# Kernel tuning notes

Hardware: AMD Instinct MI355X
Metric: run time of the kernel (lower is better)

Reference implementation:

```python
import jax, jax.numpy as jnp
import numpy as np
import math

B, S, D = 4, 4096, 1024
H = 16
HD = D // H          # head_dim = 64
M = 256              # nb_features (random projection dim)


def _orthogonal_gaussian(key, m, d):
    # FAVOR+ orthogonal random features: blocks of d orthogonal rows,
    # each row rescaled to a chi-distributed norm (norm of a d-dim gaussian).
    n_blocks = int(math.ceil(m / d))
    keys = jax.random.split(key, n_blocks + 1)
    blocks = []
    for i in range(n_blocks):
        g = jax.random.normal(keys[i], (d, d), dtype=jnp.float32)
        q, _ = jnp.linalg.qr(g)
        blocks.append(q.T)
    W = jnp.concatenate(blocks, axis=0)[:m]  # [m, d]
    norms = jnp.linalg.norm(
        jax.random.normal(keys[-1], (m, d), dtype=jnp.float32), axis=1, keepdims=True)
    return W * norms


def _softmax_kernel(x, proj, is_query, eps=1e-4):
    # x: [b,h,s,d]; proj: [m,d]. Standard FAVOR+ positive softmax features.
    d = x.shape[-1]
    ratio = proj.shape[0] ** -0.5
    x = x * (d ** -0.25)
    u = jnp.einsum('bhsd,md->bhsm', x, proj)  # projection
    diag = 0.5 * jnp.sum(x * x, axis=-1, keepdims=True)  # [b,h,s,1]
    if is_query:
        stab = jnp.max(u, axis=-1, keepdims=True)
    else:
        stab = jnp.max(u, axis=(-1, -2), keepdims=True)
    return ratio * (jnp.exp(u - diag - stab) + eps)


def performer_attention(Q, K, V, mask, proj):
    # Q,K,V: [b,h,s,d], mask: [b,s]
    scale = HD ** -0.25
    m4 = mask[:, None, :, None]
    Qs = Q * scale
    Ks = K * scale * m4
    Vs = V * m4
    q_prime = _softmax_kernel(Qs, proj, is_query=True)   # [b,h,s,m]
    k_prime = _softmax_kernel(Ks, proj, is_query=False)  # [b,h,s,m]
    # linear attention: O(s*m*d)
    kv = jnp.einsum('bhsm,bhsd->bhmd', k_prime, Vs)      # [b,h,m,d]
    z = 1.0 / (jnp.einsum('bhsm,bhm->bhs', q_prime, jnp.sum(k_prime, axis=2)) + 1e-6)
    out = jnp.einsum('bhsm,bhmd->bhsd', q_prime, kv) * z[..., None]
    return out


def setup_inputs() -> dict:
    key = jax.random.key(0)
    ks = jax.random.split(key, 9)
    X = jax.random.normal(ks[0], (B, S, D), dtype=jnp.float32)
    mask = jnp.ones((B, S), dtype=jnp.float32)
    s = D ** -0.5
    Wq = jax.random.normal(ks[1], (D, D), dtype=jnp.float32) * s
    bq = jnp.zeros((D,), dtype=jnp.float32)
    Wk = jax.random.normal(ks[2], (D, D), dtype=jnp.float32) * s
    bk = jnp.zeros((D,), dtype=jnp.float32)
    Wv = jax.random.normal(ks[3], (D, D), dtype=jnp.float32) * s
    bv = jnp.zeros((D,), dtype=jnp.float32)
    proj = _orthogonal_gaussian(ks[4], M, HD)
    return {"X": X, "mask": mask, "Wq": Wq, "bq": bq, "Wk": Wk, "bk": bk,
            "Wv": Wv, "bv": bv, "proj": proj}


def _split_heads(x):
    b, s, _ = x.shape
    return x.reshape(b, s, H, HD).transpose(0, 2, 1, 3)


def reference(X, mask, Wq, bq, Wk, bk, Wv, bv, proj):
    Q = _split_heads(X @ Wq + bq)
    K = _split_heads(X @ Wk + bk)
    V = _split_heads(X @ Wv + bv)
    attn = performer_attention(Q, K, V, mask, proj)  # [b,h,s,hd]
    out = attn.transpose(0, 2, 1, 3).reshape(B, S, D)
    return out
```

## Files before the change

### kernel.cpp

```cpp
#include <hip/hip_runtime.h>
#include <stdint.h>

#define DEVI static __device__ __forceinline__

typedef unsigned short u16;
typedef unsigned int u32;
typedef __attribute__((ext_vector_type(8))) short short8;
typedef __attribute__((ext_vector_type(4))) float f32x4;
typedef __attribute__((ext_vector_type(4))) unsigned short ushort4_t;

#define BB 4
#define SS 4096
#define DD 1024
#define HH 16
#define HDD 64
#define MM 256
#define BHN 64

DEVI u16 f2bf(float f) {
    u32 u = __float_as_uint(f);
    u += 0x7fffu + ((u >> 16) & 1u);
    return (u16)(u >> 16);
}
DEVI float bf2f(u16 h) { return __uint_as_float(((u32)h) << 16); }

typedef __attribute__((address_space(1))) const unsigned int as1_u32;
typedef __attribute__((address_space(3))) unsigned int as3_u32;
DEVI void load_lds16(const void* g, void* lds) {
    __builtin_amdgcn_global_load_lds((as1_u32*)g, (as3_u32*)lds, 16, 0, 0);
}


__global__ void conv_bf16(const float* __restrict__ src, u16* __restrict__ dst, int n4) {
    int i = blockIdx.x * 256 + threadIdx.x;
    if (i < n4) {
        float4 v = reinterpret_cast<const float4*>(src)[i];
        ushort4_t o = { f2bf(v.x), f2bf(v.y), f2bf(v.z), f2bf(v.w) };
        reinterpret_cast<ushort4_t*>(dst)[i] = o;
    }
}

__global__ void conv_w(const float* __restrict__ Wq, const float* __restrict__ Wk,
                       const float* __restrict__ Wv, u16* __restrict__ Wt) {
    __shared__ float tile[64][65];
    const int jt = blockIdx.x, kt = blockIdx.y;
    const float* src = (jt < 16) ? Wq : (jt < 32) ? Wk : Wv;
    const int j0 = (jt & 15) * 64, k0 = kt * 64;
    const int t = threadIdx.x;
    for (int i = 0; i < 16; ++i) {
        int lin = t + i * 256;
        int kl = lin >> 6, jl = lin & 63;
        tile[kl][jl] = src[(size_t)(k0 + kl) * DD + j0 + jl];
    }
    __syncthreads();
    const int jg0 = jt * 64;
    for (int i = 0; i < 16; ++i) {
        int lin = t + i * 256;
        int jl = lin >> 6, kl = lin & 63;
        Wt[(size_t)(jg0 + jl) * DD + k0 + kl] = f2bf(tile[kl][jl]);
    }
}

__global__ __launch_bounds__(512, 2) void gemm1_big(
    const u16* __restrict__ Xbf, const u16* __restrict__ Wt,
    const float* __restrict__ bq, const float* __restrict__ bk, const float* __restrict__ bv,
    const float* __restrict__ mask,
    u16* __restrict__ Qh, u16* __restrict__ Kh, u16* __restrict__ Vt,
    float* __restrict__ dq, float* __restrict__ dk)
{
    extern __shared__ __align__(16) char smem[];
    const int tid = threadIdx.x, l = tid & 63, wv = tid >> 6;
    const int wm = wv >> 2, wn = wv & 3;
    const int bid = blockIdx.x;
    const int xcd = bid & 7, i6 = bid >> 3;
    const int bx = xcd * 8 + i6 / 12, by = i6 % 12;
    const int row0 = bx * 256, col0 = by * 256;

    const int srow = tid >> 3;
    const int scol = ((tid & 7) ^ (srow & 7)) * 8;

    #define ABUF(p) ((char*)smem + (p) * 32768)
    #define BBUF(p) ((char*)smem + 65536 + (p) * 32768)
    #define STA(p, kt, r) load_lds16(Xbf + (size_t)(row0 + (r)*64 + srow) * DD + (kt)*64 + scol, \
                                     ABUF(p) + (r)*8192 + wv*1024)
    #define STB(p, kt, r) load_lds16(Wt + (size_t)(col0 + (r)*64 + srow) * DD + (kt)*64 + scol, \
                                     BBUF(p) + (r)*8192 + wv*1024)

    STA(0,0,0); STA(0,0,1); STA(0,0,2); STA(0,0,3);
    STB(0,0,0); STB(0,0,1); STB(0,0,2); STB(0,0,3);
    asm volatile("s_waitcnt vmcnt(0)" ::: "memory");
    __builtin_amdgcn_s_barrier();
    __builtin_amdgcn_sched_barrier(0);

    f32x4 acc[8][4] = {};
    const int arow_b = wm * 128 + (l & 15);
    const int brow_b = wn * 64 + (l & 15);
    const int cb_b = (l >> 4) * 16;
    const int lx = (l & 7) << 4;

    for (int kt = 0; kt < 16; ++kt) {
        const int p = kt & 1, pn = p ^ 1;
        const bool more = (kt + 1) < 16;
        short8 bfr[4][2];
#pragma unroll
        for (int q = 0; q < 4; ++q) {
            if (more) {
                if (q == 0)      { STA(pn, kt + 1, 0); STA(pn, kt + 1, 1); }
                else if (q == 1) { STA(pn, kt + 1, 2); STA(pn, kt + 1, 3); }
                else if (q == 2) { STB(pn, kt + 1, 0); STB(pn, kt + 1, 1); }
                else             { STB(pn, kt + 1, 2); STB(pn, kt + 1, 3); }
            }
            if (q == 0) {
#pragma unroll
                for (int nf = 0; nf < 4; ++nf) {
                    const int br = brow_b + nf * 16;
#pragma unroll
                    for (int ks = 0; ks < 2; ++ks)
                        bfr[nf][ks] = *(const short8*)(BBUF(p) + br * 128 + ((cb_b + ks * 64) ^ lx));
                }
            }
            short8 a[2][2];
#pragma unroll
            for (int i = 0; i < 2; ++i) {
                const int ar = arow_b + (q * 2 + i) * 16;
#pragma unroll
                for (int ks = 0; ks < 2; ++ks)
                    a[i][ks] = *(const short8*)(ABUF(p) + ar * 128 + ((cb_b + ks * 64) ^ lx));
            }
            __builtin_amdgcn_s_setprio(1);
#pragma unroll
            for (int i = 0; i < 2; ++i)
#pragma unroll
                for (int nf = 0; nf < 4; ++nf) {
                    acc[q*2+i][nf] = __builtin_amdgcn_mfma_f32_16x16x32_bf16(a[i][0], bfr[nf][0], acc[q*2+i][nf], 0, 0, 0);
                    acc[q*2+i][nf] = __builtin_amdgcn_mfma_f32_16x16x32_bf16(a[i][1], bfr[nf][1], acc[q*2+i][nf], 0, 0, 0);
                }
            __builtin_amdgcn_s_setprio(0);
            __builtin_amdgcn_sched_barrier(0);
        }
        asm volatile("s_waitcnt vmcnt(0)" ::: "memory");
        __builtin_amdgcn_s_barrier();
        __builtin_amdgcn_sched_barrier(0);
    }

    const int region = by >> 2;
    const int h = ((by & 3) << 2) + wn;
    const int rg = row0 + wm * 128;
    const int b = rg >> 12;
    const int sb = rg & 4095;
    const size_t bh = (size_t)(b * HH + h);
    const int dd = l & 15;
    const int jbase = ((by & 3) << 8) + wn * 64;

    if (region == 0) {
        float bias[4];
#pragma unroll
        for (int nf = 0; nf < 4; ++nf) bias[nf] = bq[jbase + nf * 16 + dd];
#pragma unroll
        for (int mf = 0; mf < 8; ++mf) {
            float ds4[4];
#pragma unroll
            for (int g = 0; g < 4; ++g) {
                const int s = sb + mf * 16 + ((l >> 4) << 2) + g;
                float dsum = 0.f;
#pragma unroll
                for (int nf = 0; nf < 4; ++nf) {
                    u16 hv = f2bf((acc[mf][nf][g] + bias[nf]) * 0.125f);
                    Qh[(bh * SS + s) * HDD + nf * 16 + dd] = hv;
                    float fv = bf2f(hv);
                    dsum += fv * fv;
                }
                dsum += __shfl_xor(dsum, 1);
                dsum += __shfl_xor(dsum, 2);
                dsum += __shfl_xor(dsum, 4);
                dsum += __shfl_xor(dsum, 8);
                ds4[g] = 0.5f * dsum;
            }
            if (dd == 0)
                *(float4*)(dq + bh * SS + sb + mf * 16 + ((l >> 4) << 2)) =
                    make_float4(ds4[0], ds4[1], ds4[2], ds4[3]);
        }
    } else if (region == 1) {
        float bias[4];
#pragma unroll
        for (int nf = 0; nf < 4; ++nf) bias[nf] = bk[jbase + nf * 16 + dd];
#pragma unroll
        for (int mf = 0; mf < 8; ++mf) {
            float ds4[4];
#pragma unroll
            for (int g = 0; g < 4; ++g) {
                const int s = sb + mf * 16 + ((l >> 4) << 2) + g;
                const float m = mask[b * SS + s];
                float dsum = 0.f;
#pragma unroll
                for (int nf = 0; nf < 4; ++nf) {
                    u16 hv = f2bf((acc[mf][nf][g] + bias[nf]) * m * 0.125f);
                    Kh[(bh * SS + s) * HDD + nf * 16 + dd] = hv;
                    float fv = bf2f(hv);
                    dsum += fv * fv;
                }
                dsum += __shfl_xor(dsum, 1);
                dsum += __shfl_xor(dsum, 2);
                dsum += __shfl_xor(dsum, 4);
                dsum += __shfl_xor(dsum, 8);
                ds4[g] = 0.5f * dsum;
            }
            if (dd == 0)
                *(float4*)(dk + bh * SS + sb + mf * 16 + ((l >> 4) << 2)) =
                    make_float4(ds4[0], ds4[1], ds4[2], ds4[3]);
        }
    } else {
        float bias[4];
#pragma unroll
        for (int nf = 0; nf < 4; ++nf) bias[nf] = bv[jbase + nf * 16 + dd];
#pragma unroll
        for (int mf = 0; mf < 8; ++mf) {
            const int s0 = sb + mf * 16 + ((l >> 4) << 2);
#pragma unroll
            for (int nf = 0; nf < 4; ++nf) {
                ushort4_t pk;
#pragma unroll
                for (int g = 0; g < 4; ++g) {
                    const float m = mask[b * SS + s0 + g];
                    pk[g] = f2bf((acc[mf][nf][g] + bias[nf]) * m);
                }
                *(ushort4_t*)(Vt + (bh * HDD + nf * 16 + dd) * SS + s0) = pk;
            }
        }
    }
    #undef ABUF
    #undef BBUF
    #undef STA
    #undef STB
}

__global__ __launch_bounds__(256, 2) void kv_fused(
    const u16* __restrict__ Kh, const u16* __restrict__ Vt,
    const u16* __restrict__ projb, const float* __restrict__ dk,
    float* __restrict__ kv_part, float* __restrict__ ksum_part,
    float* __restrict__ vsum_part, float* __restrict__ lstab)
{
    extern __shared__ __align__(16) char ksm[];
    #define KLDS(b) ((char*)ksm + (b) * 8192)
    #define VLDS(b) ((char*)ksm + 24576 + (b) * 8192)
    u16* Kp = (u16*)((char*)ksm + 49152);
    const int tid = threadIdx.x, l = tid & 63, wv = tid >> 6;
    const int ck = blockIdx.x, bh = blockIdx.y;
    short8 pb[4][2];
#pragma unroll
    for (int nf = 0; nf < 4; ++nf)
#pragma unroll
        for (int ks = 0; ks < 2; ++ks)
            pb[nf][ks] = *(const short8*)(projb + (wv * 64 + nf * 16 + (l & 15)) * HDD + ks * 32 + (l >> 4) * 8);
    const size_t sbase = (size_t)bh * SS + ck * 512;

    #define KSTAGE(buf, it8) do { \
        const int s0_ = (it8) * 64; \
        _Pragma("unroll") \
        for (int c = 0; c < 2; ++c) { \
            const int rb = wv * 16 + c * 8; \
            const int r = rb + (l >> 3); \
            const int sc = ((l & 7) ^ (r & 7)) * 8; \
            load_lds16(Kh + (sbase + s0_ + r) * HDD + sc, KLDS(buf) + rb * 128); \
        } \
    } while (0)
    #define VSTAGE(buf, it8) do { \
        const int s0_ = (it8) * 64; \
        _Pragma("unroll") \
        for (int c = 0; c < 2; ++c) { \
            const int rb = wv * 16 + c * 8; \
            const int r = rb + (l >> 3); \
            const int sc = ((l & 7) ^ (r & 7)) * 8; \
            load_lds16(Vt + ((size_t)bh * HDD + r) * SS + ck * 512 + s0_ + sc, VLDS(buf) + rb * 128); \
        } \
    } while (0)

    float wmax = -3.0e38f;
    KSTAGE(0, 0);
    for (int it = 0; it < 8; ++it) {
        if (it + 1 < 8) {
            KSTAGE((it + 1) % 3, it + 1);
            asm volatile("s_waitcnt vmcnt(2)" ::: "memory");
        } else {
            asm volatile("s_waitcnt vmcnt(0)" ::: "memory");
        }
        __syncthreads();
        const int bs = it % 3;
#pragma unroll
        for (int sf = 0; sf < 4; ++sf) {
            const int s = sf * 16 + (l & 15);
            f32x4 u4[4] = {};
#pragma unroll
            for (int ks = 0; ks < 2; ++ks) {
                short8 ak = *(const short8*)(KLDS(bs) + s * 128 + ((ks * 64 + (l >> 4) * 16) ^ ((s & 7) << 4)));
#pragma unroll
                for (int nf = 0; nf < 4; ++nf)
                    u4[nf] = __builtin_amdgcn_mfma_f32_16x16x32_bf16(ak, pb[nf][ks], u4[nf], 0, 0, 0);
            }
#pragma unroll
            for (int nf = 0; nf < 4; ++nf)
#pragma unroll
                for (int g = 0; g < 4; ++g) wmax = fmaxf(wmax, u4[nf][g]);
        }
    }
#pragma unroll
    for (int o = 1; o < 64; o <<= 1) wmax = fmaxf(wmax, __shfl_xor(wmax, o));
    if (l == 0) lstab[((size_t)ck * BHN + bh) * 4 + wv] = wmax;
    const float stab = wmax;

    f32x4 acc[4][4] = {};
    float ksc[4] = {0.f, 0.f, 0.f, 0.f};
    float vsc[4] = {0.f, 0.f, 0.f, 0.f};
    KSTAGE(0, 0); VSTAGE(0, 0);
    for (int it = 0; it < 8; ++it) {
        if (it + 1 < 8) {
            KSTAGE((it + 1) % 3, it + 1);
            VSTAGE((it + 1) % 3, it + 1);
            asm volatile("s_waitcnt vmcnt(4)" ::: "memory");
        } else {
            asm volatile("s_waitcnt vmcnt(0)" ::: "memory");
        }
        __syncthreads();
        const int bs = it % 3;
        const int s0 = it * 64;
#pragma unroll
        for (int sf = 0; sf < 4; ++sf) {
            const int s = sf * 16 + (l & 15);
            f32x4 u4[4] = {};
#pragma unroll
            for (int ks = 0; ks < 2; ++ks) {
                short8 ak = *(const short8*)(KLDS(bs) + s * 128 + ((ks * 64 + (l >> 4) * 16) ^ ((s & 7) << 4)));
#pragma unroll
                for (int nf = 0; nf < 4; ++nf)
                    u4[nf] = __builtin_amdgcn_mfma_f32_16x16x32_bf16(ak, pb[nf][ks], u4[nf], 0, 0, 0);
            }
            const int srow = sf * 16 + (l >> 4) * 4;
            const float4 dkv = *(const float4*)(dk + sbase + s0 + srow);
#pragma unroll
            for (int nf = 0; nf < 4; ++nf) {
                const int m = wv * 64 + nf * 16 + (l & 15);
                u16 h0 = f2bf(__expf(u4[nf][0] - dkv.x - stab));
                u16 h1 = f2bf(__expf(u4[nf][1] - dkv.y - stab));
                u16 h2 = f2bf(__expf(u4[nf][2] - dkv.z - stab));
                u16 h3 = f2bf(__expf(u4[nf][3] - dkv.w - stab));
                ksc[nf] += bf2f(h0) + bf2f(h1) + bf2f(h2) + bf2f(h3);
                uint2 w; w.x = (u32)h0 | ((u32)h1 << 16); w.y = (u32)h2 | ((u32)h3 << 16);
                *(uint2*)((char*)Kp + m * 128 + ((srow * 2) ^ ((m & 7) << 4))) = w;
            }
        }
        __syncthreads();
#pragma unroll
        for (int ks = 0; ks < 2; ++ks) {
            short8 am[4], bv8[4];
#pragma unroll
            for (int mf = 0; mf < 4; ++mf) {
                const int m = wv * 64 + mf * 16 + (l & 15);
                am[mf] = *(const short8*)((const char*)Kp + m * 128 + ((ks * 64 + (l >> 4) * 16) ^ ((m & 7) << 4)));
            }
#pragma unroll
            for (int nf = 0; nf < 4; ++nf) {
                const int d = nf * 16 + (l & 15);
                bv8[nf] = *(const short8*)(VLDS(bs) + d * 128 + ((ks * 64 + (l >> 4) * 16) ^ ((d & 7) << 4)));
                float vs = 0.f;
#pragma unroll
                for (int e = 0; e < 8; ++e) vs += bf2f((u16)bv8[nf][e]);
                vsc[nf] += vs;
            }
#pragma unroll
            for (int mf = 0; mf < 4; ++mf)
#pragma unroll
                for (int nf = 0; nf < 4; ++nf)
                    acc[mf][nf] = __builtin_amdgcn_mfma_f32_16x16x32_bf16(am[mf], bv8[nf], acc[mf][nf], 0, 0, 0);
        }
    }
    const size_t pbase = (size_t)ck * BHN + bh;
#pragma unroll
    for (int nf = 0; nf < 4; ++nf) {
        float v = ksc[nf];
        v += __shfl_xor(v, 16);
        v += __shfl_xor(v, 32);
        if (l < 16) ksum_part[pbase * MM + wv * 64 + nf * 16 + l] = v;
        float w = vsc[nf];
        w += __shfl_xor(w, 16);
        w += __shfl_xor(w, 32);
        if (wv == 0 && l < 16) vsum_part[pbase * HDD + nf * 16 + l] = w;
    }
#pragma unroll
    for (int mf = 0; mf < 4; ++mf)
#pragma unroll
        for (int nf = 0; nf < 4; ++nf)
            *(f32x4*)(kv_part + (pbase * HDD + nf * 16 + (l & 15)) * MM + wv * 64 + mf * 16 + (l >> 4) * 4) = acc[mf][nf];
    #undef KLDS
    #undef VLDS
    #undef KSTAGE
    #undef VSTAGE
}

__global__ void reduceB3(const float* __restrict__ kv_part, const float* __restrict__ ksum_part,
                         const float* __restrict__ vsum_part, const float* __restrict__ lstab,
                         u16* __restrict__ Bmat) {
    __shared__ float f[8][4];
    const int bh = blockIdx.x, n = blockIdx.y, t = threadIdx.x;
    if (t < 32) {
        float lv = lstab[((size_t)(t >> 2) * BHN + bh) * 4 + (t & 3)];
        float g = lv;
#pragma unroll
        for (int o = 1; o < 32; o <<= 1) g = fmaxf(g, __shfl_xor(g, o));
        f[t >> 2][t & 3] = __expf(lv - g);
    }
    __syncthreads();
    const int grp = t >> 6;
    float s = 0.f;
    if (n < 64) {
        float vsg = 0.f;
#pragma unroll
        for (int ck = 0; ck < 8; ++ck) {
            vsg += vsum_part[((size_t)ck * BHN + bh) * HDD + n];
            s += kv_part[(((size_t)ck * BHN + bh) * HDD + n) * MM + t] * f[ck][grp];
        }
        s = 0.0625f * (s + 1e-4f * vsg);
    } else if (n == 64) {
#pragma unroll
        for (int ck = 0; ck < 8; ++ck)
            s += ksum_part[((size_t)ck * BHN + bh) * MM + t] * f[ck][grp];
        s = 0.0625f * (s + 1e-4f * 4096.0f);
    }
    Bmat[((size_t)bh * 80 + n) * MM + t] = (n <= 64) ? f2bf(s) : (u16)0;
}

__global__ __launch_bounds__(256) void out_fused(
    const u16* __restrict__ Qh, const u16* __restrict__ projb,
    const float* __restrict__ dq, const u16* __restrict__ Bmat,
    float* __restrict__ out)
{
    __shared__ __align__(16) u16 Qlds[64 * 64];
    __shared__ __align__(16) u16 qlds[64 * 256];
    __shared__ float red[4][64];
    const int tid = threadIdx.x, l = tid & 63, wv = tid >> 6;
    const int rt = blockIdx.x, bh = blockIdx.y;
    const size_t srowbase = (size_t)bh * SS + rt * 64;
#pragma unroll
    for (int c = 0; c < 2; ++c) {
        const int rb = wv * 16 + c * 8;
        const int r = rb + (l >> 3);
        load_lds16(Qh + (srowbase + r) * HDD + (((l & 7) ^ (r & 7)) * 8), (char*)Qlds + rb * 128);
    }
    short8 pa[4][2];
#pragma unroll
    for (int mf = 0; mf < 4; ++mf)
#pragma unroll
        for (int ks = 0; ks < 2; ++ks)
            pa[mf][ks] = *(const short8*)(projb + (wv * 64 + mf * 16 + (l & 15)) * HDD + ks * 32 + (l >> 4) * 8);
    __syncthreads();
    f32x4 u[4][4] = {};
#pragma unroll
    for (int ks = 0; ks < 2; ++ks) {
        short8 bq8[4];
#pragma unroll
        for (int nf = 0; nf < 4; ++nf) {
            const int s = nf * 16 + (l & 15);
            bq8[nf] = *(const short8*)((const char*)Qlds + s * 128 + ((ks * 64 + (l >> 4) * 16) ^ ((s & 7) << 4)));
        }
#pragma unroll
        for (int mf = 0; mf < 4; ++mf)
#pragma unroll
            for (int nf = 0; nf < 4; ++nf)
                u[mf][nf] = __builtin_amdgcn_mfma_f32_16x16x32_bf16(pa[mf][ks], bq8[nf], u[mf][nf], 0, 0, 0);
    }
#pragma unroll
    for (int nf = 0; nf < 4; ++nf) {
        float v = -3.0e38f;
#pragma unroll
        for (int mf = 0; mf < 4; ++mf)
#pragma unroll
            for (int g = 0; g < 4; ++g) v = fmaxf(v, u[mf][nf][g]);
        v = fmaxf(v, __shfl_xor(v, 16));
        v = fmaxf(v, __shfl_xor(v, 32));
        if ((l >> 4) == 0) red[wv][nf * 16 + l] = v;
    }
    __syncthreads();
#pragma unroll
    for (int nf = 0; nf < 4; ++nf) {
        const int s = nf * 16 + (l & 15);
        const float mx = fmaxf(fmaxf(red[0][s], red[1][s]), fmaxf(red[2][s], red[3][s]));
        const float dg = dq[srowbase + s];
#pragma unroll
        for (int mf = 0; mf < 4; ++mf) {
            u16 h0 = f2bf(0.0625f * (__expf(u[mf][nf][0] - dg - mx) + 1e-4f));
            u16 h1 = f2bf(0.0625f * (__expf(u[mf][nf][1] - dg - mx) + 1e-4f));
            u16 h2 = f2bf(0.0625f * (__expf(u[mf][nf][2] - dg - mx) + 1e-4f));
            u16 h3 = f2bf(0.0625f * (__expf(u[mf][nf][3] - dg - mx) + 1e-4f));
            uint2 w; w.x = (u32)h0 | ((u32)h1 << 16); w.y = (u32)h2 | ((u32)h3 << 16);
            const int mb = (wv * 64 + mf * 16 + (l >> 4) * 4) * 2;
            *(uint2*)((char*)qlds + s * 512 + (mb ^ ((s & 7) << 4))) = w;
        }
    }
    __syncthreads();
    const u16* bbase = Bmat + (size_t)bh * 20480;
    f32x4 acc[4][2] = {};
#pragma unroll
    for (int kt = 0; kt < 8; ++kt) {
        short8 aq[4], bb[2];
#pragma unroll
        for (int mf = 0; mf < 4; ++mf) {
            const int s = mf * 16 + (l & 15);
            aq[mf] = *(const short8*)((const char*)qlds + s * 512 + ((kt * 64 + (l >> 4) * 16) ^ ((s & 7) << 4)));
        }
        bb[0] = *(const short8*)(bbase + (wv * 16 + (l & 15)) * 256 + kt * 32 + (l >> 4) * 8);
        bb[1] = *(const short8*)(bbase + (64 + (l & 15)) * 256 + kt * 32 + (l >> 4) * 8);
#pragma unroll
        for (int mf = 0; mf < 4; ++mf)
#pragma unroll
            for (int nf = 0; nf < 2; ++nf)
                acc[mf][nf] = __builtin_amdgcn_mfma_f32_16x16x32_bf16(aq[mf], bb[nf], acc[mf][nf], 0, 0, 0);
    }
    const int b = bh >> 4, h = bh & 15;
#pragma unroll
    for (int mf = 0; mf < 4; ++mf) {
#pragma unroll
        for (int g = 0; g < 4; ++g) {
            const float den = __shfl(acc[mf][1][g], (l & 48));
            const float z = 1.0f / (den + 1e-6f);
            const int s = rt * 64 + mf * 16 + (l >> 4) * 4 + g;
            out[((size_t)b * SS + s) * DD + h * HDD + wv * 16 + (l & 15)] = acc[mf][0][g] * z;
        }
    }
}

extern "C" void kernel_launch(void* const* d_in, const int* in_sizes, int n_in,
                              void* d_out, int out_size, void* d_ws, size_t ws_size,
                              hipStream_t stream)
{
    const float* X    = (const float*)d_in[0];
    const float* mask = (const float*)d_in[1];
    const float* Wq   = (const float*)d_in[2];
    const float* bq   = (const float*)d_in[3];
    const float* Wk   = (const float*)d_in[4];
    const float* bk   = (const float*)d_in[5];
    const float* Wv   = (const float*)d_in[6];
    const float* bv   = (const float*)d_in[7];
    const float* proj = (const float*)d_in[8];
    float* out = (float*)d_out;

    char* p = (char*)d_ws;
    u16* Xbf = (u16*)p;
    float* kv_part = (float*)p; p += 33554432;
    u16* Wt = (u16*)p;    p += 6291456;
    u16* projb = (u16*)p; p += 32768;
    u16* Qh = (u16*)p;    p += 33554432;
    u16* Kh = (u16*)p;    p += 33554432;
    u16* Vt = (u16*)p;    p += 33554432;
    float* dq = (float*)p; p += 1048576;
    float* dk = (float*)p; p += 1048576;
    float* ksum_part = (float*)p; p += 524288;
    u16* Bmat = (u16*)p;  p += 2621440;
    float* vsum_part = (float*)p; p += 131072;
    float* lstab = (float*)p; p += 8192;
    if (ws_size < 145924096ull) return;

    hipFuncSetAttribute((const void*)gemm1_big, hipFuncAttributeMaxDynamicSharedMemorySize, 131072);
    hipFuncSetAttribute((const void*)kv_fused, hipFuncAttributeMaxDynamicSharedMemorySize, 81920);

    conv_bf16<<<16384, 256, 0, stream>>>(X, Xbf, 4194304);
    conv_w<<<dim3(48, 16), 256, 0, stream>>>(Wq, Wk, Wv, Wt);
    conv_bf16<<<16, 256, 0, stream>>>(proj, projb, 4096);
    gemm1_big<<<768, 512, 131072, stream>>>(Xbf, Wt, bq, bk, bv, mask, Qh, Kh, Vt, dq, dk);
    kv_fused<<<dim3(8, 64), 256, 81920, stream>>>(Kh, Vt, projb, dk, kv_part, ksum_part, vsum_part, lstab);
    reduceB3<<<dim3(64, 80), 256, 0, stream>>>(kv_part, ksum_part, vsum_part, lstab, Bmat);
    out_fused<<<dim3(64, 64), 256, 0, stream>>>(Qh, projb, dq, Bmat, out);
}
```

Baseline: 260.1 us.

## Rework QKV GEMM prefetch schedule and use online max in K-feature pass

The projection GEMM now prefetches A tiles two k-steps ahead and issues one B stage per phase, with 4x2 MFMA sub-tiles and barriers around each phase. The goal is to hide more global-load latency. Separately, the kv_fused kernel drops its first pass over K that found the global max. It now keeps a running max per chunk and rescales the accumulators and key sums whenever the max grows, so the K projection MFMAs and K loads happen once instead of twice. The cost is extra per-phase barriers in the GEMM, plus possible rescale work and more register pressure from holding all 16 u4 tiles.

New measurement: 268.8 us. 3.3% more time.

```diff
diff --git a/kernel.cpp b/kernel.cpp
--- a/kernel.cpp
+++ b/kernel.cpp
@@ -61,7 +61,7 @@
     }
 }
 
-__global__ __launch_bounds__(512, 2) void gemm1_big(
+__global__ __launch_bounds__(512, 2) void gemm1_m8(
     const u16* __restrict__ Xbf, const u16* __restrict__ Wt,
     const float* __restrict__ bq, const float* __restrict__ bk, const float* __restrict__ bv,
     const float* __restrict__ mask,
@@ -88,7 +88,8 @@
 
     STA(0,0,0); STA(0,0,1); STA(0,0,2); STA(0,0,3);
     STB(0,0,0); STB(0,0,1); STB(0,0,2); STB(0,0,3);
-    asm volatile("s_waitcnt vmcnt(0)" ::: "memory");
+    STA(1,1,0); STA(1,1,1); STA(1,1,2); STA(1,1,3);
+    asm volatile("s_waitcnt vmcnt(4)" ::: "memory");
     __builtin_amdgcn_s_barrier();
     __builtin_amdgcn_sched_barrier(0);
 
@@ -100,45 +101,50 @@
 
     for (int kt = 0; kt < 16; ++kt) {
         const int p = kt & 1, pn = p ^ 1;
-        const bool more = (kt + 1) < 16;
-        short8 bfr[4][2];
-#pragma unroll
-        for (int q = 0; q < 4; ++q) {
-            if (more) {
-                if (q == 0)      { STA(pn, kt + 1, 0); STA(pn, kt + 1, 1); }
-                else if (q == 1) { STA(pn, kt + 1, 2); STA(pn, kt + 1, 3); }
-                else if (q == 2) { STB(pn, kt + 1, 0); STB(pn, kt + 1, 1); }
-                else             { STB(pn, kt + 1, 2); STB(pn, kt + 1, 3); }
-            }
-            if (q == 0) {
-#pragma unroll
-                for (int nf = 0; nf < 4; ++nf) {
-                    const int br = brow_b + nf * 16;
+        const bool haveN = (kt + 1) < 16;
+        short8 bfr[2][2];
+#pragma unroll
+        for (int ph = 0; ph < 4; ++ph) {
+            const int mh = ph & 1, nh = ph >> 1;
+            if (haveN) STB(pn, kt + 1, ph);
+            if (mh == 0) {
+#pragma unroll
+                for (int j = 0; j < 2; ++j) {
+                    const int br = brow_b + (nh * 2 + j) * 16;
 #pragma unroll
                     for (int ks = 0; ks < 2; ++ks)
-                        bfr[nf][ks] = *(const short8*)(BBUF(p) + br * 128 + ((cb_b + ks * 64) ^ lx));
+                        bfr[j][ks] = *(const short8*)(BBUF(p) + br * 128 + ((cb_b + ks * 64) ^ lx));
                 }
             }
-            short8 a[2][2];
-#pragma unroll
-            for (int i = 0; i < 2; ++i) {
-                const int ar = arow_b + (q * 2 + i) * 16;
+            short8 a[4][2];
+#pragma unroll
+            for (int i = 0; i < 4; ++i) {
+                const int ar = arow_b + (mh * 4 + i) * 16;
 #pragma unroll
                 for (int ks = 0; ks < 2; ++ks)
                     a[i][ks] = *(const short8*)(ABUF(p) + ar * 128 + ((cb_b + ks * 64) ^ lx));
             }
+            __builtin_amdgcn_s_barrier();
+            asm volatile("s_waitcnt lgkmcnt(0)" ::: "memory");
+            __builtin_amdgcn_sched_barrier(0);
             __builtin_amdgcn_s_setprio(1);
 #pragma unroll
-            for (int i = 0; i < 2; ++i)
-#pragma unroll
-                for (int nf = 0; nf < 4; ++nf) {
-                    acc[q*2+i][nf] = __builtin_amdgcn_mfma_f32_16x16x32_bf16(a[i][0], bfr[nf][0], acc[q*2+i][nf], 0, 0, 0);
-                    acc[q*2+i][nf] = __builtin_amdgcn_mfma_f32_16x16x32_bf16(a[i][1], bfr[nf][1], acc[q*2+i][nf], 0, 0, 0);
+            for (int i = 0; i < 4; ++i)
+#pragma unroll
+                for (int j = 0; j < 2; ++j) {
+                    acc[mh*4+i][nh*2+j] = __builtin_amdgcn_mfma_f32_16x16x32_bf16(a[i][0], bfr[j][0], acc[mh*4+i][nh*2+j], 0, 0, 0);
+                    acc[mh*4+i][nh*2+j] = __builtin_amdgcn_mfma_f32_16x16x32_bf16(a[i][1], bfr[j][1], acc[mh*4+i][nh*2+j], 0, 0, 0);
                 }
             __builtin_amdgcn_s_setprio(0);
             __builtin_amdgcn_sched_barrier(0);
-        }
-        asm volatile("s_waitcnt vmcnt(0)" ::: "memory");
+            __builtin_amdgcn_s_barrier();
+        }
+        if (kt + 2 < 16) {
+            STA(p, kt + 2, 0); STA(p, kt + 2, 1); STA(p, kt + 2, 2); STA(p, kt + 2, 3);
+            asm volatile("s_waitcnt vmcnt(4)" ::: "memory");
+        } else {
+            asm volatile("s_waitcnt vmcnt(0)" ::: "memory");
+        }
         __builtin_amdgcn_s_barrier();
         __builtin_amdgcn_sched_barrier(0);
     }
@@ -275,39 +281,7 @@
         } \
     } while (0)
 
-    float wmax = -3.0e38f;
-    KSTAGE(0, 0);
-    for (int it = 0; it < 8; ++it) {
-        if (it + 1 < 8) {
-            KSTAGE((it + 1) % 3, it + 1);
-            asm volatile("s_waitcnt vmcnt(2)" ::: "memory");
-        } else {
-            asm volatile("s_waitcnt vmcnt(0)" ::: "memory");
-        }
-        __syncthreads();
-        const int bs = it % 3;
-#pragma unroll
-        for (int sf = 0; sf < 4; ++sf) {
-            const int s = sf * 16 + (l & 15);
-            f32x4 u4[4] = {};
-#pragma unroll
-            for (int ks = 0; ks < 2; ++ks) {
-                short8 ak = *(const short8*)(KLDS(bs) + s * 128 + ((ks * 64 + (l >> 4) * 16) ^ ((s & 7) << 4)));
-#pragma unroll
-                for (int nf = 0; nf < 4; ++nf)
-                    u4[nf] = __builtin_amdgcn_mfma_f32_16x16x32_bf16(ak, pb[nf][ks], u4[nf], 0, 0, 0);
-            }
-#pragma unroll
-            for (int nf = 0; nf < 4; ++nf)
-#pragma unroll
-                for (int g = 0; g < 4; ++g) wmax = fmaxf(wmax, u4[nf][g]);
-        }
-    }
-#pragma unroll
-    for (int o = 1; o < 64; o <<= 1) wmax = fmaxf(wmax, __shfl_xor(wmax, o));
-    if (l == 0) lstab[((size_t)ck * BHN + bh) * 4 + wv] = wmax;
-    const float stab = wmax;
-
+    float mrun = -3.0e38f;
     f32x4 acc[4][4] = {};
     float ksc[4] = {0.f, 0.f, 0.f, 0.f};
     float vsc[4] = {0.f, 0.f, 0.f, 0.f};
@@ -323,26 +297,52 @@
         __syncthreads();
         const int bs = it % 3;
         const int s0 = it * 64;
+        f32x4 u4[4][4];
 #pragma unroll
         for (int sf = 0; sf < 4; ++sf) {
+#pragma unroll
+            for (int nf = 0; nf < 4; ++nf) u4[sf][nf] = (f32x4){0.f, 0.f, 0.f, 0.f};
             const int s = sf * 16 + (l & 15);
-            f32x4 u4[4] = {};
 #pragma unroll
             for (int ks = 0; ks < 2; ++ks) {
                 short8 ak = *(const short8*)(KLDS(bs) + s * 128 + ((ks * 64 + (l >> 4) * 16) ^ ((s & 7) << 4)));
 #pragma unroll
                 for (int nf = 0; nf < 4; ++nf)
-                    u4[nf] = __builtin_amdgcn_mfma_f32_16x16x32_bf16(ak, pb[nf][ks], u4[nf], 0, 0, 0);
-            }
+                    u4[sf][nf] = __builtin_amdgcn_mfma_f32_16x16x32_bf16(ak, pb[nf][ks], u4[sf][nf], 0, 0, 0);
+            }
+        }
+        float pmax = -3.0e38f;
+#pragma unroll
+        for (int sf = 0; sf < 4; ++sf)
+#pragma unroll
+            for (int nf = 0; nf < 4; ++nf)
+#pragma unroll
+                for (int g = 0; g < 4; ++g) pmax = fmaxf(pmax, u4[sf][nf][g]);
+#pragma unroll
+        for (int o = 1; o < 64; o <<= 1) pmax = fmaxf(pmax, __shfl_xor(pmax, o));
+        if (pmax > mrun) {
+            const float fac = __expf(mrun - pmax);
+            mrun = pmax;
+#pragma unroll
+            for (int mf = 0; mf < 4; ++mf)
+#pragma unroll
+                for (int nf = 0; nf < 4; ++nf)
+#pragma unroll
+                    for (int g = 0; g < 4; ++g) acc[mf][nf][g] *= fac;
+#pragma unroll
+            for (int nf = 0; nf < 4; ++nf) ksc[nf] *= fac;
+        }
+#pragma unroll
+        for (int sf = 0; sf < 4; ++sf) {
             const int srow = sf * 16 + (l >> 4) * 4;
             const float4 dkv = *(const float4*)(dk + sbase + s0 + srow);
 #pragma unroll
             for (int nf = 0; nf < 4; ++nf) {
                 const int m = wv * 64 + nf * 16 + (l & 15);
-                u16 h0 = f2bf(__expf(u4[nf][0] - dkv.x - stab));
-                u16 h1 = f2bf(__expf(u4[nf][1] - dkv.y - stab));
-                u16 h2 = f2bf(__expf(u4[nf][2] - dkv.z - stab));
-                u16 h3 = f2bf(__expf(u4[nf][3] - dkv.w - stab));
+                u16 h0 = f2bf(__expf(u4[sf][nf][0] - dkv.x - mrun));
+                u16 h1 = f2bf(__expf(u4[sf][nf][1] - dkv.y - mrun));
+                u16 h2 = f2bf(__expf(u4[sf][nf][2] - dkv.z - mrun));
+                u16 h3 = f2bf(__expf(u4[sf][nf][3] - dkv.w - mrun));
                 ksc[nf] += bf2f(h0) + bf2f(h1) + bf2f(h2) + bf2f(h3);
                 uint2 w; w.x = (u32)h0 | ((u32)h1 << 16); w.y = (u32)h2 | ((u32)h3 << 16);
                 *(uint2*)((char*)Kp + m * 128 + ((srow * 2) ^ ((m & 7) << 4))) = w;
@@ -373,6 +373,7 @@
                     acc[mf][nf] = __builtin_amdgcn_mfma_f32_16x16x32_bf16(am[mf], bv8[nf], acc[mf][nf], 0, 0, 0);
         }
     }
+    if (l == 0) lstab[((size_t)ck * BHN + bh) * 4 + wv] = mrun;
     const size_t pbase = (size_t)ck * BHN + bh;
 #pragma unroll
     for (int nf = 0; nf < 4; ++nf) {
@@ -558,13 +559,13 @@
     float* lstab = (float*)p; p += 8192;
     if (ws_size < 145924096ull) return;
 
-    hipFuncSetAttribute((const void*)gemm1_big, hipFuncAttributeMaxDynamicSharedMemorySize, 131072);
+    hipFuncSetAttribute((const void*)gemm1_m8, hipFuncAttributeMaxDynamicSharedMemorySize, 131072);
     hipFuncSetAttribute((const void*)kv_fused, hipFuncAttributeMaxDynamicSharedMemorySize, 81920);
 
     conv_bf16<<<16384, 256, 0, stream>>>(X, Xbf, 4194304);
     conv_w<<<dim3(48, 16), 256, 0, stream>>>(Wq, Wk, Wv, Wt);
     conv_bf16<<<16, 256, 0, stream>>>(proj, projb, 4096);
-    gemm1_big<<<768, 512, 131072, stream>>>(Xbf, Wt, bq, bk, bv, mask, Qh, Kh, Vt, dq, dk);
+    gemm1_m8<<<768, 512, 131072, stream>>>(Xbf, Wt, bq, bk, bv, mask, Qh, Kh, Vt, dq, dk);
     kv_fused<<<dim3(8, 64), 256, 81920, stream>>>(Kh, Vt, projb, dk, kv_part, ksum_part, vsum_part, lstab);
     reduceB3<<<dim3(64, 80), 256, 0, stream>>>(kv_part, ksum_part, vsum_part, lstab, Bmat);
     out_fused<<<dim3(64, 64), 256, 0, stream>>>(Qh, projb, dq, Bmat, out);
```
